# Kernel tuning notes

Hardware: AMD Instinct MI355X
Metric: run time of the kernel (lower is better)

Reference implementation:

```python
import jax, jax.numpy as jnp
import numpy as np

NS, NH, NL, NP, E = 2, 8, 4, 4, 256
HD = E // NH  # 32


def grid_sample_zeros(img, grid):
    """torch.F.grid_sample(mode='bilinear', padding_mode='zeros', align_corners=False).
    img: [B, C, Hs, Ws]; grid: [B, Hg, Wg, 2] with (x, y) in [-1, 1]. Returns [B, C, Hg, Wg]."""
    B, C, Hs, Ws = img.shape
    gx = (grid[..., 0] + 1.0) * (Ws * 0.5) - 0.5  # pixel-space x
    gy = (grid[..., 1] + 1.0) * (Hs * 0.5) - 0.5  # pixel-space y
    x0 = jnp.floor(gx)
    y0 = jnp.floor(gy)
    x1, y1 = x0 + 1.0, y0 + 1.0
    wx1 = gx - x0
    wx0 = 1.0 - wx1
    wy1 = gy - y0
    wy0 = 1.0 - wy1
    imgf = img.reshape(B, C, Hs * Ws)

    def gather(ix, iy):
        valid = (ix >= 0) & (ix < Ws) & (iy >= 0) & (iy < Hs)
        ixc = jnp.clip(ix, 0, Ws - 1).astype(jnp.int32)
        iyc = jnp.clip(iy, 0, Hs - 1).astype(jnp.int32)
        flat = (iyc * Ws + ixc).reshape(B, 1, -1)
        vals = jnp.take_along_axis(imgf, flat, axis=2).reshape(B, C, *ix.shape[1:])
        return vals * valid[:, None].astype(img.dtype)

    return (gather(x0, y0) * (wx0 * wy0)[:, None]
            + gather(x1, y0) * (wx1 * wy0)[:, None]
            + gather(x0, y1) * (wx0 * wy1)[:, None]
            + gather(x1, y1) * (wx1 * wy1)[:, None])


def setup_inputs() -> dict:
    key = jax.random.key(0)
    ks = jax.random.split(key, 10)
    bs, Q = 2048, NL * NP  # num_query forced to num_levels*num_points = 16
    f = jnp.float32
    s = 1.0 / np.sqrt(E)
    return {
        "query": jax.random.normal(ks[0], (bs, Q, E), f),
        "key_hist": jax.random.normal(ks[1], (bs, Q, E), f),
        "value_hist": jax.random.normal(ks[2], (bs, Q, E), f),
        "reference_points": jax.random.uniform(ks[3], (bs, Q, NL, 2), f),
        "spatial_shapes": jnp.full((NL, 2), 2, dtype=jnp.int32),  # each level 2x2, sum HW = 16
        "Wq": jax.random.normal(ks[4], (E, E), f) * s, "bq": jnp.zeros((E,), f),
        "Wk": jax.random.normal(ks[5], (E, E), f) * s, "bk": jnp.zeros((E,), f),
        "Wv": jax.random.normal(ks[6], (E, E), f) * s, "bv": jnp.zeros((E,), f),
        "Woff": jax.random.normal(ks[7], (E, NH * NL * NP * 2), f) * (0.01 * s), "boff": jnp.zeros((NH * NL * NP * 2,), f),
        "Wout": jax.random.normal(ks[8], (E, E), f) * s, "bout": jnp.zeros((E,), f),
    }


def reference(query, key_hist, value_hist, reference_points, spatial_shapes,
              Wq, bq, Wk, bk, Wv, bv, Woff, boff, Wout, bout):
    bs, Q, _ = query.shape
    B = bs * NS
    residual = query

    # torch cat(dim=1)+view interleaves the two sequences per batch: index 2b -> query, 2b+1 -> hist
    queries = jnp.repeat(query, NS, axis=0)                              # [B, Q, E]
    keys = jnp.stack([query, key_hist], axis=1).reshape(B, Q, E)
    values = jnp.stack([query, value_hist], axis=1).reshape(B, Q, E)
    rp = jnp.repeat(reference_points, NS, axis=0)                        # [B, Q, NL, 2] (both copies identical)

    qh = (queries @ Wq + bq).reshape(B, Q, NH, HD)
    kh = (keys @ Wk + bk).reshape(B, Q, NH, HD)
    vh = (values @ Wv + bv).reshape(B, Q, NH, HD)

    attn = jax.nn.softmax(jnp.einsum('bqhd,bkhd->bqhk', qh, kh), axis=-1)
    attn = attn.reshape(B, Q, NH, NL, NP)

    offsets = (queries @ Woff + boff).reshape(B, Q, NH, NL, NP, 2)
    norm = jnp.stack([spatial_shapes[:, 1], spatial_shapes[:, 0]], axis=-1).astype(query.dtype)  # (W, H)
    loc = rp[:, :, None, :, None, :] + offsets / norm[None, None, None, :, None, :]
    grid = 2.0 * loc - 1.0                                               # [B, Q, NH, NL, NP, 2]

    ss = np.asarray(spatial_shapes)                                      # static level shapes
    attw = attn.transpose(0, 2, 1, 3, 4).reshape(B * NH, Q, NL, NP)      # [BH, Q, NL, NP]
    acc = jnp.zeros((B * NH, HD, Q), dtype=query.dtype)
    start = 0
    for l in range(NL):
        H_, W_ = int(ss[l, 0]), int(ss[l, 1])
        hw = H_ * W_
        v_l = vh[:, start:start + hw].transpose(0, 2, 3, 1).reshape(B * NH, HD, H_, W_)
        g_l = grid[:, :, :, l].transpose(0, 2, 1, 3, 4).reshape(B * NH, Q, NP, 2)
        s_l = grid_sample_zeros(v_l, g_l)                                # [BH, HD, Q, NP]
        acc = acc + jnp.sum(s_l * attw[:, None, :, l, :], axis=-1)       # weighted reduce over points
        start += hw

    out = acc.reshape(B, E, Q).transpose(0, 2, 1)                        # [B, Q, E]
    out = out.reshape(bs, NS, Q, E).mean(axis=1)                         # mean over the two sequences
    return out @ Wout + bout + residual                                  # dropout is identity in eval
```

## Files before the change

### kernel.cpp

```cpp
#include <hip/hip_runtime.h>

typedef float  f32x4  __attribute__((ext_vector_type(4)));
typedef __bf16 bf16x8 __attribute__((ext_vector_type(8)));
typedef __bf16 bf16x4 __attribute__((ext_vector_type(4)));

__device__ __forceinline__ bf16x8 cvt8(float4 a, float4 b) {
    bf16x8 r;
    r[0] = (__bf16)a.x; r[1] = (__bf16)a.y; r[2] = (__bf16)a.z; r[3] = (__bf16)a.w;
    r[4] = (__bf16)b.x; r[5] = (__bf16)b.y; r[6] = (__bf16)b.z; r[7] = (__bf16)b.w;
    return r;
}

#define OF_OFF 524288
#define PV_OFF (1u << 20)

__global__ void wprep(const float* __restrict__ Wq, const float* __restrict__ Wk,
                      const float* __restrict__ Wv, const float* __restrict__ Woff,
                      const float* __restrict__ Wout, __bf16* __restrict__ ws) {
    int id = blockIdx.x * 256 + threadIdx.x;
    if (id < 262144) {
        int tile = id >> 9, e = id & 511;
        int lane = e >> 3, j = e & 7;
        int kt = tile & 7, nh = (tile >> 3) & 1, mat = (tile >> 4) & 3, h = tile >> 6;
        int k = kt * 32 + (lane >> 4) * 8 + j;
        int col = h * 32 + nh * 16 + (lane & 15);
        const float* W = (mat == 0) ? Wq : (mat == 1) ? Wk : (mat == 2) ? Wv : Woff;
        ws[id] = (__bf16)W[k * 256 + col];
    } else {
        int i = id - 262144;
        int tile = i >> 9, e = i & 511;
        int lane = e >> 3, j = e & 7;
        int kt = tile & 7, nt = tile >> 3;
        int k = kt * 32 + (lane >> 4) * 8 + j;
        int col = nt * 16 + (lane & 15);
        ws[262144 + i] = (__bf16)Wout[k * 256 + col];
    }
}

__launch_bounds__(512, 4)
__global__ void tsa_one(const float* __restrict__ query, const float* __restrict__ keyh,
                        const float* __restrict__ valh, const float* __restrict__ refpts,
                        unsigned char* __restrict__ wsw,
                        const float* __restrict__ bq, const float* __restrict__ bk,
                        const float* __restrict__ bv, const float* __restrict__ boff,
                        const float* __restrict__ bout, float* __restrict__ out, int b0)
{
    __shared__ __attribute__((aligned(16))) unsigned char uni[16384];
    __shared__ __attribute__((aligned(16))) unsigned char scr_all[24576];
    __shared__ __attribute__((aligned(16))) unsigned char vfr[32768];
    const int t = threadIdx.x;
    const int lane = t & 63, w = t >> 6, l15 = lane & 15, lhi = lane >> 4;
    const int p = w >> 1;
    const int role = w & 1;
    const long b = (long)b0 + (long)blockIdx.x * 4 + p;
    unsigned char* scrp = scr_all + p * 6144;
    unsigned char* vfrp = vfr + p * 8192;
    __bf16* pvg = (__bf16*)(wsw + PV_OFF) + ((long)blockIdx.x * 4 + p) * 4096;

    bf16x8 afr[8];
    {
        const float* s0 = (role ? keyh : query) + b * 4096 + l15 * 256;
        #pragma unroll
        for (int kt = 0; kt < 8; ++kt) {
            int o = kt * 32 + lhi * 8;
            afr[kt] = cvt8(*(const float4*)(s0 + o), *(const float4*)(s0 + o + 4));
        }
        if (role) {
            const float* s1 = valh + b * 4096 + l15 * 256;
            #pragma unroll
            for (int kt = 0; kt < 8; ++kt) {
                int o = kt * 32 + lhi * 8;
                *(bf16x8*)(vfrp + kt * 1024 + lane * 16) =
                    cvt8(*(const float4*)(s1 + o), *(const float4*)(s1 + o + 4));
            }
        }
    }
    const f32x4 z = (f32x4){0.f, 0.f, 0.f, 0.f};
    __syncthreads();

    for (int h = 0; h < 8; ++h) {
        #pragma unroll 2
        for (int nh = 0; nh < 2; ++nh) {
            f32x4 acc[4];
            #pragma unroll
            for (int i = 0; i < 4; ++i) acc[i] = z;
            #pragma unroll 2
            for (int half = 0; half < 2; ++half) {
                __syncthreads();
                #pragma unroll
                for (int it = 0; it < 2; ++it) {
                    int u = t + it * 512;
                    int f = u >> 6;
                    int kt = (half << 2) + (f & 3);
                    const void* src = (const void*)(wsw +
                        ((((h * 4 + (f >> 2)) * 2 + nh) * 8 + kt) << 10) + (u & 63) * 16);
                    __builtin_amdgcn_global_load_lds(
                        (const __attribute__((address_space(1))) unsigned int*)src,
                        (__attribute__((address_space(3))) unsigned int*)(uni + u * 16),
                        16, 0, 0);
                }
                __syncthreads();
                #pragma unroll
                for (int ktl = 0; ktl < 4; ++ktl) {
                    int kt = (half << 2) + ktl;
                    const unsigned char* bb = uni + ktl * 1024 + lane * 16;
                    bf16x8 b_k = *(const bf16x8*)(bb + 4096);
                    bf16x8 b_v = *(const bf16x8*)(bb + 8192);
                    if (!role) {
                        bf16x8 b_q = *(const bf16x8*)(bb);
                        bf16x8 b_o = *(const bf16x8*)(bb + 12288);
                        acc[0] = __builtin_amdgcn_mfma_f32_16x16x32_bf16(afr[kt], b_q, acc[0], 0, 0, 0);
                        acc[1] = __builtin_amdgcn_mfma_f32_16x16x32_bf16(afr[kt], b_k, acc[1], 0, 0, 0);
                        acc[2] = __builtin_amdgcn_mfma_f32_16x16x32_bf16(afr[kt], b_v, acc[2], 0, 0, 0);
                        acc[3] = __builtin_amdgcn_mfma_f32_16x16x32_bf16(afr[kt], b_o, acc[3], 0, 0, 0);
                    } else {
                        bf16x8 av = *(const bf16x8*)(vfrp + kt * 1024 + lane * 16);
                        acc[0] = __builtin_amdgcn_mfma_f32_16x16x32_bf16(afr[kt], b_k, acc[0], 0, 0, 0);
                        acc[1] = __builtin_amdgcn_mfma_f32_16x16x32_bf16(av,      b_v, acc[1], 0, 0, 0);
                    }
                }
            }
            {
                int dcol = nh * 16 + l15;
                int gcol = h * 32 + dcol;
                if (!role) {
                    float bqv = bq[gcol], bkv = bk[gcol], bvv = bv[gcol], bov = boff[gcol];
                    #pragma unroll
                    for (int r = 0; r < 4; ++r) {
                        int row = lhi * 4 + r;
                        *(__bf16*)(scrp + row * 64 + dcol * 2)        = (__bf16)(acc[0][r] + bqv);
                        *(__bf16*)(scrp + 1024 + row * 64 + dcol * 2) = (__bf16)(acc[1][r] + bkv);
                        *(__bf16*)(scrp + 3072 + dcol * 64 + row * 2) = (__bf16)(acc[2][r] + bvv);
                        *(__bf16*)(scrp + 5120 + row * 64 + dcol * 2) = (__bf16)(acc[3][r] + bov);
                    }
                } else {
                    float bkv = bk[gcol], bvv = bv[gcol];
                    #pragma unroll
                    for (int r = 0; r < 4; ++r) {
                        int row = lhi * 4 + r;
                        *(__bf16*)(scrp + 2048 + row * 64 + dcol * 2)      = (__bf16)(acc[0][r] + bkv);
                        *(__bf16*)(scrp + 3072 + dcol * 64 + 32 + row * 2) = (__bf16)(acc[1][r] + bvv);
                    }
                }
            }
        }
        __syncthreads();

        bf16x8 qf = *(const bf16x8*)(scrp + l15 * 64 + lhi * 16);
        bf16x8 kf = *(const bf16x8*)(scrp + 1024 + role * 1024 + l15 * 64 + lhi * 16);
        f32x4 S = __builtin_amdgcn_mfma_f32_16x16x32_bf16(kf, qf, z, 0, 0, 0);
        float pr[4];
        {
            float m = fmaxf(fmaxf(S[0], S[1]), fmaxf(S[2], S[3]));
            m = fmaxf(m, __shfl_xor(m, 16)); m = fmaxf(m, __shfl_xor(m, 32));
            float s = 0.f;
            #pragma unroll
            for (int r = 0; r < 4; ++r) { pr[r] = __expf(S[r] - m); s += pr[r]; }
            s += __shfl_xor(s, 16); s += __shfl_xor(s, 32);
            float inv = 1.f / s;
            #pragma unroll
            for (int r = 0; r < 4; ++r) pr[r] *= inv;
        }

        {
            float2 rp = *(const float2*)(refpts + b * 128 + l15 * 8 + lhi * 2);
            bf16x8 off8 = *(const bf16x8*)(scrp + 5120 + l15 * 64 + lhi * 16);
            float w4[4] = {0.f, 0.f, 0.f, 0.f};
            #pragma unroll
            for (int pp = 0; pp < 4; ++pp) {
                float gx = 2.f * rp.x + (float)off8[2 * pp]     - 0.5f;
                float gy = 2.f * rp.y + (float)off8[2 * pp + 1] - 0.5f;
                float tx0 = fmaxf(0.f, 1.f - fabsf(gx));
                float tx1 = fmaxf(0.f, 1.f - fabsf(gx - 1.f));
                float ty0 = fmaxf(0.f, 1.f - fabsf(gy));
                float ty1 = fmaxf(0.f, 1.f - fabsf(gy - 1.f));
                w4[0] += tx0 * ty0 * pr[pp]; w4[1] += tx1 * ty0 * pr[pp];
                w4[2] += tx0 * ty1 * pr[pp]; w4[3] += tx1 * ty1 * pr[pp];
            }
            *(bf16x4*)(scrp + 1024 + role * 1024 + l15 * 64 + lhi * 8) =
                (bf16x4){(__bf16)w4[0], (__bf16)w4[1], (__bf16)w4[2], (__bf16)w4[3]};
        }
        __syncthreads();

        {
            bf16x8 aW = *(const bf16x8*)(scrp + 1024 + (lhi >> 1) * 1024 + l15 * 64 + (lhi & 1) * 16);
            bf16x8 vf = *(const bf16x8*)(scrp + 3072 + (role * 16 + l15) * 64 + lhi * 16);
            f32x4 c = __builtin_amdgcn_mfma_f32_16x16x32_bf16(aW, vf, z, 0, 0, 0);
            #pragma unroll
            for (int r = 0; r < 4; ++r) {
                int qq = lhi * 4 + r;
                *(__bf16*)(scrp + qq * 64 + (role * 16 + l15) * 2) = (__bf16)(0.5f * c[r]);
            }
        }
        __syncthreads();
        if (!role) {
            bf16x8 pvfrag = *(const bf16x8*)(scrp + l15 * 64 + lhi * 16);
            *(bf16x8*)(pvg + h * 512 + lane * 8) = pvfrag;
        }
    }

    __syncthreads();

    {
        bf16x8 pv[8];
        #pragma unroll
        for (int kt = 0; kt < 8; ++kt)
            pv[kt] = *(const bf16x8*)(pvg + kt * 512 + lane * 8);
        for (int qd = 0; qd < 4; ++qd) {
            f32x4 o2[2];
            o2[0] = z; o2[1] = z;
            #pragma unroll
            for (int kt = 0; kt < 8; ++kt) {
                #pragma unroll
                for (int j = 0; j < 2; ++j) {
                    int ntl = role * 2 + j;
                    bf16x8 bfr = *(const bf16x8*)(wsw + OF_OFF + qd * 32768 +
                                                  (ntl * 8 + kt) * 1024 + lane * 16);
                    o2[j] = __builtin_amdgcn_mfma_f32_16x16x32_bf16(pv[kt], bfr, o2[j], 0, 0, 0);
                }
            }
            #pragma unroll
            for (int j = 0; j < 2; ++j) {
                int ntl = role * 2 + j;
                int col = (qd * 4 + ntl) * 16 + l15;
                float bo = bout[col];
                #pragma unroll
                for (int r = 0; r < 4; ++r) {
                    int qq = lhi * 4 + r;
                    long idx = b * 4096 + qq * 256 + col;
                    out[idx] = o2[j][r] + bo + query[idx];
                }
            }
        }
    }
}

extern "C" void kernel_launch(void* const* d_in, const int* in_sizes, int n_in,
                              void* d_out, int out_size, void* d_ws, size_t ws_size,
                              hipStream_t stream) {
    const float* query      = (const float*)d_in[0];
    const float* key_hist   = (const float*)d_in[1];
    const float* value_hist = (const float*)d_in[2];
    const float* refpts     = (const float*)d_in[3];
    const float* Wq   = (const float*)d_in[5];
    const float* bq   = (const float*)d_in[6];
    const float* Wk   = (const float*)d_in[7];
    const float* bk   = (const float*)d_in[8];
    const float* Wv   = (const float*)d_in[9];
    const float* bv   = (const float*)d_in[10];
    const float* Woff = (const float*)d_in[11];
    const float* boff = (const float*)d_in[12];
    const float* Wout = (const float*)d_in[13];
    const float* bout = (const float*)d_in[14];
    float* outp = (float*)d_out;

    const int bs = in_sizes[0] / 4096;
    wprep<<<1280, 256, 0, stream>>>(Wq, Wk, Wv, Woff, Wout, (__bf16*)d_ws);

    long avail = (long)ws_size - (long)PV_OFF;
    int CB = bs;
    if (avail < (long)bs * 8192) {
        CB = (int)(avail / 8192) & ~3;
        if (CB < 4) CB = 4;
    }
    for (int b0 = 0; b0 < bs; b0 += CB) {
        int nb = (bs - b0 < CB ? bs - b0 : CB) / 4;
        tsa_one<<<nb, 512, 0, stream>>>(query, key_hist, value_hist, refpts,
                                        (unsigned char*)d_ws,
                                        bq, bk, bv, boff, bout, outp, b0);
    }
}
```

Measured before the change: 86.35 us.

## Double-buffer weight tiles in LDS and keep value fragments in registers

```diff
diff --git a/kernel.cpp b/kernel.cpp
--- a/kernel.cpp
+++ b/kernel.cpp
@@ -37,6 +37,22 @@
     }
 }
 
+__device__ __forceinline__ void stage_issue(const unsigned char* wsw, int h, int nh, int half,
+                                            unsigned char* buf, int t) {
+    #pragma unroll
+    for (int it = 0; it < 2; ++it) {
+        int u = t + it * 512;
+        int f = u >> 6;
+        int kt = half * 4 + (f & 3);
+        const void* src = (const void*)(wsw +
+            ((((h * 4 + (f >> 2)) * 2 + nh) * 8 + kt) << 10) + (u & 63) * 16);
+        __builtin_amdgcn_global_load_lds(
+            (const __attribute__((address_space(1))) unsigned int*)src,
+            (__attribute__((address_space(3))) unsigned int*)(buf + u * 16),
+            16, 0, 0);
+    }
+}
+
 __launch_bounds__(512, 4)
 __global__ void tsa_one(const float* __restrict__ query, const float* __restrict__ keyh,
                         const float* __restrict__ valh, const float* __restrict__ refpts,
@@ -45,19 +61,21 @@
                         const float* __restrict__ bv, const float* __restrict__ boff,
                         const float* __restrict__ bout, float* __restrict__ out, int b0)
 {
-    __shared__ __attribute__((aligned(16))) unsigned char uni[16384];
+    __shared__ __attribute__((aligned(16))) unsigned char uni[32768];
     __shared__ __attribute__((aligned(16))) unsigned char scr_all[24576];
-    __shared__ __attribute__((aligned(16))) unsigned char vfr[32768];
     const int t = threadIdx.x;
     const int lane = t & 63, w = t >> 6, l15 = lane & 15, lhi = lane >> 4;
     const int p = w >> 1;
     const int role = w & 1;
     const long b = (long)b0 + (long)blockIdx.x * 4 + p;
     unsigned char* scrp = scr_all + p * 6144;
-    unsigned char* vfrp = vfr + p * 8192;
+    unsigned char* buf0 = uni;
+    unsigned char* buf1 = uni + 16384;
     __bf16* pvg = (__bf16*)(wsw + PV_OFF) + ((long)blockIdx.x * 4 + p) * 4096;
 
     bf16x8 afr[8];
+    bf16x8 avc[4];
+    const float* vp = valh + b * 4096 + l15 * 256;
     {
         const float* s0 = (role ? keyh : query) + b * 4096 + l15 * 256;
         #pragma unroll
@@ -66,84 +84,91 @@
             afr[kt] = cvt8(*(const float4*)(s0 + o), *(const float4*)(s0 + o + 4));
         }
         if (role) {
-            const float* s1 = valh + b * 4096 + l15 * 256;
-            #pragma unroll
-            for (int kt = 0; kt < 8; ++kt) {
-                int o = kt * 32 + lhi * 8;
-                *(bf16x8*)(vfrp + kt * 1024 + lane * 16) =
-                    cvt8(*(const float4*)(s1 + o), *(const float4*)(s1 + o + 4));
+            #pragma unroll
+            for (int ktl = 0; ktl < 4; ++ktl) {
+                int o = ktl * 32 + lhi * 8;
+                avc[ktl] = cvt8(*(const float4*)(vp + o), *(const float4*)(vp + o + 4));
             }
         }
     }
     const f32x4 z = (f32x4){0.f, 0.f, 0.f, 0.f};
+
+    auto do_half = [&](const unsigned char* buf, int half, f32x4* acc) {
+        #pragma unroll
+        for (int ktl = 0; ktl < 4; ++ktl) {
+            int kt = half * 4 + ktl;
+            const unsigned char* bb = buf + ktl * 1024 + lane * 16;
+            bf16x8 b_k = *(const bf16x8*)(bb + 4096);
+            bf16x8 b_v = *(const bf16x8*)(bb + 8192);
+            if (!role) {
+                bf16x8 b_q = *(const bf16x8*)(bb);
+                bf16x8 b_o = *(const bf16x8*)(bb + 12288);
+                acc[0] = __builtin_amdgcn_mfma_f32_16x16x32_bf16(afr[kt], b_q, acc[0], 0, 0, 0);
+                acc[1] = __builtin_amdgcn_mfma_f32_16x16x32_bf16(afr[kt], b_k, acc[1], 0, 0, 0);
+                acc[2] = __builtin_amdgcn_mfma_f32_16x16x32_bf16(afr[kt], b_v, acc[2], 0, 0, 0);
+                acc[3] = __builtin_amdgcn_mfma_f32_16x16x32_bf16(afr[kt], b_o, acc[3], 0, 0, 0);
+            } else {
+                acc[0] = __builtin_amdgcn_mfma_f32_16x16x32_bf16(afr[kt], b_k, acc[0], 0, 0, 0);
+                acc[1] = __builtin_amdgcn_mfma_f32_16x16x32_bf16(avc[ktl], b_v, acc[1], 0, 0, 0);
+            }
+        }
+        if (role) {
+            int oh = (1 - half) * 4;
+            #pragma unroll
+            for (int ktl = 0; ktl < 4; ++ktl) {
+                int o = (oh + ktl) * 32 + lhi * 8;
+                avc[ktl] = cvt8(*(const float4*)(vp + o), *(const float4*)(vp + o + 4));
+            }
+        }
+    };
+
+    auto scatter = [&](int h, int nh, const f32x4* acc) {
+        int dcol = nh * 16 + l15;
+        int gcol = h * 32 + dcol;
+        if (!role) {
+            float bqv = bq[gcol], bkv = bk[gcol], bvv = bv[gcol], bov = boff[gcol];
+            #pragma unroll
+            for (int r = 0; r < 4; ++r) {
+                int row = lhi * 4 + r;
+                *(__bf16*)(scrp + row * 64 + dcol * 2)        = (__bf16)(acc[0][r] + bqv);
+                *(__bf16*)(scrp + 1024 + row * 64 + dcol * 2) = (__bf16)(acc[1][r] + bkv);
+                *(__bf16*)(scrp + 3072 + dcol * 64 + row * 2) = (__bf16)(acc[2][r] + bvv);
+                *(__bf16*)(scrp + 5120 + row * 64 + dcol * 2) = (__bf16)(acc[3][r] + bov);
+            }
+        } else {
+            float bkv = bk[gcol], bvv = bv[gcol];
+            #pragma unroll
+            for (int r = 0; r < 4; ++r) {
+                int row = lhi * 4 + r;
+                *(__bf16*)(scrp + 2048 + row * 64 + dcol * 2)      = (__bf16)(acc[0][r] + bkv);
+                *(__bf16*)(scrp + 3072 + dcol * 64 + 32 + row * 2) = (__bf16)(acc[1][r] + bvv);
+            }
+        }
+    };
+
+    stage_issue(wsw, 0, 0, 0, buf0, t);
     __syncthreads();
 
     for (int h = 0; h < 8; ++h) {
-        #pragma unroll 2
-        for (int nh = 0; nh < 2; ++nh) {
-            f32x4 acc[4];
-            #pragma unroll
-            for (int i = 0; i < 4; ++i) acc[i] = z;
-            #pragma unroll 2
-            for (int half = 0; half < 2; ++half) {
-                __syncthreads();
-                #pragma unroll
-                for (int it = 0; it < 2; ++it) {
-                    int u = t + it * 512;
-                    int f = u >> 6;
-                    int kt = (half << 2) + (f & 3);
-                    const void* src = (const void*)(wsw +
-                        ((((h * 4 + (f >> 2)) * 2 + nh) * 8 + kt) << 10) + (u & 63) * 16);
-                    __builtin_amdgcn_global_load_lds(
-                        (const __attribute__((address_space(1))) unsigned int*)src,
-                        (__attribute__((address_space(3))) unsigned int*)(uni + u * 16),
-                        16, 0, 0);
-                }
-                __syncthreads();
-                #pragma unroll
-                for (int ktl = 0; ktl < 4; ++ktl) {
-                    int kt = (half << 2) + ktl;
-                    const unsigned char* bb = uni + ktl * 1024 + lane * 16;
-                    bf16x8 b_k = *(const bf16x8*)(bb + 4096);
-                    bf16x8 b_v = *(const bf16x8*)(bb + 8192);
-                    if (!role) {
-                        bf16x8 b_q = *(const bf16x8*)(bb);
-                        bf16x8 b_o = *(const bf16x8*)(bb + 12288);
-                        acc[0] = __builtin_amdgcn_mfma_f32_16x16x32_bf16(afr[kt], b_q, acc[0], 0, 0, 0);
-                        acc[1] = __builtin_amdgcn_mfma_f32_16x16x32_bf16(afr[kt], b_k, acc[1], 0, 0, 0);
-                        acc[2] = __builtin_amdgcn_mfma_f32_16x16x32_bf16(afr[kt], b_v, acc[2], 0, 0, 0);
-                        acc[3] = __builtin_amdgcn_mfma_f32_16x16x32_bf16(afr[kt], b_o, acc[3], 0, 0, 0);
-                    } else {
-                        bf16x8 av = *(const bf16x8*)(vfrp + kt * 1024 + lane * 16);
-                        acc[0] = __builtin_amdgcn_mfma_f32_16x16x32_bf16(afr[kt], b_k, acc[0], 0, 0, 0);
-                        acc[1] = __builtin_amdgcn_mfma_f32_16x16x32_bf16(av,      b_v, acc[1], 0, 0, 0);
-                    }
-                }
-            }
-            {
-                int dcol = nh * 16 + l15;
-                int gcol = h * 32 + dcol;
-                if (!role) {
-                    float bqv = bq[gcol], bkv = bk[gcol], bvv = bv[gcol], bov = boff[gcol];
-                    #pragma unroll
-                    for (int r = 0; r < 4; ++r) {
-                        int row = lhi * 4 + r;
-                        *(__bf16*)(scrp + row * 64 + dcol * 2)        = (__bf16)(acc[0][r] + bqv);
-                        *(__bf16*)(scrp + 1024 + row * 64 + dcol * 2) = (__bf16)(acc[1][r] + bkv);
-                        *(__bf16*)(scrp + 3072 + dcol * 64 + row * 2) = (__bf16)(acc[2][r] + bvv);
-                        *(__bf16*)(scrp + 5120 + row * 64 + dcol * 2) = (__bf16)(acc[3][r] + bov);
-                    }
-                } else {
-                    float bkv = bk[gcol], bvv = bv[gcol];
-                    #pragma unroll
-                    for (int r = 0; r < 4; ++r) {
-                        int row = lhi * 4 + r;
-                        *(__bf16*)(scrp + 2048 + row * 64 + dcol * 2)      = (__bf16)(acc[0][r] + bkv);
-                        *(__bf16*)(scrp + 3072 + dcol * 64 + 32 + row * 2) = (__bf16)(acc[1][r] + bvv);
-                    }
-                }
-            }
-        }
+        f32x4 acc[4];
+        #pragma unroll
+        for (int i = 0; i < 4; ++i) acc[i] = z;
+
+        stage_issue(wsw, h, 0, 1, buf1, t);
+        do_half(buf0, 0, acc);
+        __syncthreads();
+        stage_issue(wsw, h, 1, 0, buf0, t);
+        do_half(buf1, 1, acc);
+        scatter(h, 0, acc);
+        __syncthreads();
+        #pragma unroll
+        for (int i = 0; i < 4; ++i) acc[i] = z;
+        stage_issue(wsw, h, 1, 1, buf1, t);
+        do_half(buf0, 0, acc);
+        __syncthreads();
+        if (h < 7) stage_issue(wsw, h + 1, 0, 0, buf0, t);
+        do_half(buf1, 1, acc);
+        scatter(h, 1, acc);
         __syncthreads();
 
         bf16x8 qf = *(const bf16x8*)(scrp + l15 * 64 + lhi * 16);
```

After: 136.5 us. +58.0%, slower.

## Double-buffer weight staging into LDS with prefetch of next chunk

Applied to the files above, without the earlier changes.

```diff
diff --git a/kernel.cpp b/kernel.cpp
--- a/kernel.cpp
+++ b/kernel.cpp
@@ -37,6 +37,19 @@
     }
 }
 
+__device__ __forceinline__ void stage8(const unsigned char* wsw, int s,
+                                       unsigned char* buf, int t) {
+    int h = s >> 3, nh = (s >> 2) & 1, pr = s & 3;
+    int f = t >> 6;
+    int kt = pr * 2 + (f & 1);
+    const void* src = (const void*)(wsw +
+        ((((h * 4 + (f >> 1)) * 2 + nh) * 8 + kt) << 10) + (t & 63) * 16);
+    __builtin_amdgcn_global_load_lds(
+        (const __attribute__((address_space(1))) unsigned int*)src,
+        (__attribute__((address_space(3))) unsigned int*)(buf + t * 16),
+        16, 0, 0);
+}
+
 __launch_bounds__(512, 4)
 __global__ void tsa_one(const float* __restrict__ query, const float* __restrict__ keyh,
                         const float* __restrict__ valh, const float* __restrict__ refpts,
@@ -57,6 +70,8 @@
     unsigned char* vfrp = vfr + p * 8192;
     __bf16* pvg = (__bf16*)(wsw + PV_OFF) + ((long)blockIdx.x * 4 + p) * 4096;
 
+    stage8(wsw, 0, uni, t);
+
     bf16x8 afr[8];
     {
         const float* s0 = (role ? keyh : query) + b * 4096 + l15 * 256;
@@ -76,53 +91,41 @@
         }
     }
     const f32x4 z = (f32x4){0.f, 0.f, 0.f, 0.f};
+    float2 rp = *(const float2*)(refpts + b * 128 + l15 * 8 + lhi * 2);
     __syncthreads();
 
+    int cur = 0;
     for (int h = 0; h < 8; ++h) {
-        #pragma unroll 2
-        for (int nh = 0; nh < 2; ++nh) {
-            f32x4 acc[4];
-            #pragma unroll
-            for (int i = 0; i < 4; ++i) acc[i] = z;
-            #pragma unroll 2
-            for (int half = 0; half < 2; ++half) {
-                __syncthreads();
-                #pragma unroll
-                for (int it = 0; it < 2; ++it) {
-                    int u = t + it * 512;
-                    int f = u >> 6;
-                    int kt = (half << 2) + (f & 3);
-                    const void* src = (const void*)(wsw +
-                        ((((h * 4 + (f >> 2)) * 2 + nh) * 8 + kt) << 10) + (u & 63) * 16);
-                    __builtin_amdgcn_global_load_lds(
-                        (const __attribute__((address_space(1))) unsigned int*)src,
-                        (__attribute__((address_space(3))) unsigned int*)(uni + u * 16),
-                        16, 0, 0);
-                }
-                __syncthreads();
-                #pragma unroll
-                for (int ktl = 0; ktl < 4; ++ktl) {
-                    int kt = (half << 2) + ktl;
-                    const unsigned char* bb = uni + ktl * 1024 + lane * 16;
-                    bf16x8 b_k = *(const bf16x8*)(bb + 4096);
-                    bf16x8 b_v = *(const bf16x8*)(bb + 8192);
-                    if (!role) {
-                        bf16x8 b_q = *(const bf16x8*)(bb);
-                        bf16x8 b_o = *(const bf16x8*)(bb + 12288);
-                        acc[0] = __builtin_amdgcn_mfma_f32_16x16x32_bf16(afr[kt], b_q, acc[0], 0, 0, 0);
-                        acc[1] = __builtin_amdgcn_mfma_f32_16x16x32_bf16(afr[kt], b_k, acc[1], 0, 0, 0);
-                        acc[2] = __builtin_amdgcn_mfma_f32_16x16x32_bf16(afr[kt], b_v, acc[2], 0, 0, 0);
-                        acc[3] = __builtin_amdgcn_mfma_f32_16x16x32_bf16(afr[kt], b_o, acc[3], 0, 0, 0);
-                    } else {
-                        bf16x8 av = *(const bf16x8*)(vfrp + kt * 1024 + lane * 16);
-                        acc[0] = __builtin_amdgcn_mfma_f32_16x16x32_bf16(afr[kt], b_k, acc[0], 0, 0, 0);
-                        acc[1] = __builtin_amdgcn_mfma_f32_16x16x32_bf16(av,      b_v, acc[1], 0, 0, 0);
-                    }
-                }
-            }
-            {
-                int dcol = nh * 16 + l15;
-                int gcol = h * 32 + dcol;
+        f32x4 acc[4];
+        #pragma unroll
+        for (int c = 0; c < 8; ++c) {
+            const int nh = c >> 2, pr = c & 3;
+            const int snext = h * 8 + c + 1;
+            if (snext < 64) stage8(wsw, snext, uni + (cur ^ 1) * 8192, t);
+            if (pr == 0) { acc[0] = z; acc[1] = z; acc[2] = z; acc[3] = z; }
+            const unsigned char* buf = uni + cur * 8192;
+            #pragma unroll
+            for (int ktl = 0; ktl < 2; ++ktl) {
+                const int kt = pr * 2 + ktl;
+                const unsigned char* bb = buf + ktl * 1024 + lane * 16;
+                bf16x8 b_k = *(const bf16x8*)(bb + 2048);
+                bf16x8 b_v = *(const bf16x8*)(bb + 4096);
+                if (!role) {
+                    bf16x8 b_q = *(const bf16x8*)(bb);
+                    bf16x8 b_o = *(const bf16x8*)(bb + 6144);
+                    acc[0] = __builtin_amdgcn_mfma_f32_16x16x32_bf16(afr[kt], b_q, acc[0], 0, 0, 0);
+                    acc[1] = __builtin_amdgcn_mfma_f32_16x16x32_bf16(afr[kt], b_k, acc[1], 0, 0, 0);
+                    acc[2] = __builtin_amdgcn_mfma_f32_16x16x32_bf16(afr[kt], b_v, acc[2], 0, 0, 0);
+                    acc[3] = __builtin_amdgcn_mfma_f32_16x16x32_bf16(afr[kt], b_o, acc[3], 0, 0, 0);
+                } else {
+                    bf16x8 av = *(const bf16x8*)(vfrp + kt * 1024 + lane * 16);
+                    acc[0] = __builtin_amdgcn_mfma_f32_16x16x32_bf16(afr[kt], b_k, acc[0], 0, 0, 0);
+                    acc[1] = __builtin_amdgcn_mfma_f32_16x16x32_bf16(av,      b_v, acc[1], 0, 0, 0);
+                }
+            }
+            if (pr == 3) {
+                const int dcol = nh * 16 + l15;
+                const int gcol = h * 32 + dcol;
                 if (!role) {
                     float bqv = bq[gcol], bkv = bk[gcol], bvv = bv[gcol], bov = boff[gcol];
                     #pragma unroll
@@ -143,27 +146,27 @@
                     }
                 }
             }
-        }
-        __syncthreads();
+            __syncthreads();
+            cur ^= 1;
+        }
 
         bf16x8 qf = *(const bf16x8*)(scrp + l15 * 64 + lhi * 16);
         bf16x8 kf = *(const bf16x8*)(scrp + 1024 + role * 1024 + l15 * 64 + lhi * 16);
         f32x4 S = __builtin_amdgcn_mfma_f32_16x16x32_bf16(kf, qf, z, 0, 0, 0);
-        float pr[4];
+        float pr4[4];
         {
             float m = fmaxf(fmaxf(S[0], S[1]), fmaxf(S[2], S[3]));
             m = fmaxf(m, __shfl_xor(m, 16)); m = fmaxf(m, __shfl_xor(m, 32));
             float s = 0.f;
             #pragma unroll
-            for (int r = 0; r < 4; ++r) { pr[r] = __expf(S[r] - m); s += pr[r]; }
+            for (int r = 0; r < 4; ++r) { pr4[r] = __expf(S[r] - m); s += pr4[r]; }
             s += __shfl_xor(s, 16); s += __shfl_xor(s, 32);
             float inv = 1.f / s;
             #pragma unroll
-            for (int r = 0; r < 4; ++r) pr[r] *= inv;
+            for (int r = 0; r < 4; ++r) pr4[r] *= inv;
         }
 
         {
-            float2 rp = *(const float2*)(refpts + b * 128 + l15 * 8 + lhi * 2);
             bf16x8 off8 = *(const bf16x8*)(scrp + 5120 + l15 * 64 + lhi * 16);
             float w4[4] = {0.f, 0.f, 0.f, 0.f};
             #pragma unroll
@@ -174,8 +177,8 @@
                 float tx1 = fmaxf(0.f, 1.f - fabsf(gx - 1.f));
                 float ty0 = fmaxf(0.f, 1.f - fabsf(gy));
                 float ty1 = fmaxf(0.f, 1.f - fabsf(gy - 1.f));
-                w4[0] += tx0 * ty0 * pr[pp]; w4[1] += tx1 * ty0 * pr[pp];
-                w4[2] += tx0 * ty1 * pr[pp]; w4[3] += tx1 * ty1 * pr[pp];
+                w4[0] += tx0 * ty0 * pr4[pp]; w4[1] += tx1 * ty0 * pr4[pp];
+                w4[2] += tx0 * ty1 * pr4[pp]; w4[3] += tx1 * ty1 * pr4[pp];
             }
             *(bf16x4*)(scrp + 1024 + role * 1024 + l15 * 64 + lhi * 8) =
                 (bf16x4){(__bf16)w4[0], (__bf16)w4[1], (__bf16)w4[2], (__bf16)w4[3]};
@@ -185,11 +188,11 @@
         {
             bf16x8 aW = *(const bf16x8*)(scrp + 1024 + (lhi >> 1) * 1024 + l15 * 64 + (lhi & 1) * 16);
             bf16x8 vf = *(const bf16x8*)(scrp + 3072 + (role * 16 + l15) * 64 + lhi * 16);
-            f32x4 c = __builtin_amdgcn_mfma_f32_16x16x32_bf16(aW, vf, z, 0, 0, 0);
+            f32x4 c4 = __builtin_amdgcn_mfma_f32_16x16x32_bf16(aW, vf, z, 0, 0, 0);
             #pragma unroll
             for (int r = 0; r < 4; ++r) {
                 int qq = lhi * 4 + r;
-                *(__bf16*)(scrp + qq * 64 + (role * 16 + l15) * 2) = (__bf16)(0.5f * c[r]);
+                *(__bf16*)(scrp + qq * 64 + (role * 16 + l15) * 2) = (__bf16)(0.5f * c4[r]);
             }
         }
         __syncthreads();
```

Result: slower. 91.39 us (+5.8%).
